# Performance work log

Hardware: AMD Instinct MI355X
Metric: run time of the kernel (lower is better)

## Reference

```python
import jax, jax.numpy as jnp
import numpy as np

EPS = 1e-5
SLOPE = 0.2


def knn_feature(x, k):
    # x: (B,N,C) -> (B,N,k,2C) edge features: concat(neighbor - center, center)
    xx = jnp.sum(x * x, axis=-1)                      # (B,N)
    inner = jnp.einsum('bnc,bmc->bnm', x, x)          # (B,N,N)
    pair = 2.0 * inner - xx[:, :, None] - xx[:, None, :]  # negative squared dist
    idx = jax.lax.top_k(pair, k)[1]                   # (B,N,k) nearest neighbors
    nbr = jax.vmap(lambda xb, ib: xb[ib])(x, idx)     # (B,N,k,C) gather
    ctr = jnp.broadcast_to(x[:, :, None, :], nbr.shape)
    return jnp.concatenate([nbr - ctr, ctr], axis=-1)


def conv_bn_lrelu(h, w, g, b):
    # 1x1 conv == pointwise matmul; BN in training mode (batch stats, biased var)
    h = jnp.einsum('bnkc,oc->bnko', h, w)
    m = jnp.mean(h, axis=(0, 1, 2))
    v = jnp.mean(jnp.square(h - m), axis=(0, 1, 2))
    h = g * (h - m) * jax.lax.rsqrt(v + EPS) + b
    return jnp.where(h >= 0, h, SLOPE * h)


def setup_inputs() -> dict:
    key = jax.random.key(0)
    B, N, C, K, H, O = 4, 4096, 3, 20, 64, 64
    ks = jax.random.split(key, 10)
    x = jax.random.normal(ks[0], (B, N, C), dtype=jnp.float32)
    def w(kk, o, i):
        return jax.random.normal(kk, (o, i), dtype=jnp.float32) * (1.0 / np.sqrt(i))
    return {
        'x': x,
        'w1': w(ks[1], H, 2 * C),
        'w2': w(ks[2], H, H),
        'w3': w(ks[3], H, H),
        'w4': w(ks[4], H, 2 * H),
        'w5': w(ks[5], H, H),
        'w6': w(ks[6], H, H),
        'w7': w(ks[7], H, 2 * H),
        'w8': w(ks[8], H, H),
        'w9': w(ks[9], O, H),
        'gamma': jnp.ones((9, H), dtype=jnp.float32),
        'beta': jnp.zeros((9, H), dtype=jnp.float32),
        'k': 20,
    }


def reference(x, w1, w2, w3, w4, w5, w6, w7, w8, w9, gamma, beta, k):
    h = knn_feature(x, k)                      # (B,N,k,6)
    h = conv_bn_lrelu(h, w1, gamma[0], beta[0])
    h = conv_bn_lrelu(h, w2, gamma[1], beta[1])
    h = conv_bn_lrelu(h, w3, gamma[2], beta[2])
    x1 = jnp.max(h, axis=2)                    # (B,N,64)
    h = knn_feature(x1, k)                     # (B,N,k,128)
    h = conv_bn_lrelu(h, w4, gamma[3], beta[3])
    h = conv_bn_lrelu(h, w5, gamma[4], beta[4])
    h = conv_bn_lrelu(h, w6, gamma[5], beta[5])
    x2 = jnp.max(h, axis=2)                    # (B,N,64)
    h = knn_feature(x2, k)                     # (B,N,k,128)
    h = conv_bn_lrelu(h, w7, gamma[6], beta[6])
    h = conv_bn_lrelu(h, w8, gamma[7], beta[7])
    h = conv_bn_lrelu(h, w9, gamma[8], beta[8])
    x3 = jnp.max(h, axis=2)                    # (B,N,out_features)
    return x3
```

## Files before the change

### kernel.cpp

```cpp
#include <hip/hip_runtime.h>

namespace {

constexpr int Bc   = 4;
constexpr int Nc   = 4096;
constexpr int Kc   = 20;
constexpr int BNc  = Bc * Nc;
constexpr int PIXc = BNc * Kc;
constexpr float  NEGINF = -3.0e38f;
constexpr double EPSD   = (double)1e-5f;

template<int C>
__global__ __launch_bounds__(256)
void compute_xx_xla(const float* __restrict__ X, float* __restrict__ xxf) {
    int i = blockIdx.x * 256 + threadIdx.x;
    if (i >= BNc) return;
    const float* xp = X + (size_t)i * C;
    if constexpr (C == 3) {
        const float q0 = __fmul_rn(xp[0], xp[0]);
        const float q1 = __fmul_rn(xp[1], xp[1]);
        const float q2 = __fmul_rn(xp[2], xp[2]);
        xxf[i] = __fadd_rn(__fadd_rn(q0, q1), q2);
    } else {
        float acc[16];
#pragma unroll
        for (int l = 0; l < 16; ++l) acc[l] = 0.f;
#pragma unroll
        for (int blk = 0; blk < 4; ++blk)
#pragma unroll
            for (int l = 0; l < 16; ++l)
                acc[l] = __fadd_rn(acc[l], __fmul_rn(xp[blk * 16 + l], xp[blk * 16 + l]));
        float a8[8];
#pragma unroll
        for (int l = 0; l < 8; ++l) a8[l] = __fadd_rn(acc[l], acc[l + 8]);
        float a4[4];
#pragma unroll
        for (int l = 0; l < 4; ++l) a4[l] = __fadd_rn(a8[l], a8[l + 4]);
        xxf[i] = __fadd_rn(__fadd_rn(a4[0], a4[2]), __fadd_rn(a4[1], a4[3]));
    }
}

template<int C>
__global__ __launch_bounds__(256)
void pair_tile(const float* __restrict__ X, const float* __restrict__ xxf,
               float* __restrict__ S, int b) {
    constexpr int P = C + 1;
    __shared__ float sxn[64 * P], sxm[64 * P];
    __shared__ float sxxn[64], sxxm[64];
    const int tid = threadIdx.x;
    const int tn  = blockIdx.x >> 6;
    const int tm  = blockIdx.x & 63;
    const float* Xn = X + ((size_t)b * Nc + tn * 64) * C;
    const float* Xm = X + ((size_t)b * Nc + tm * 64) * C;
    for (int f = tid; f < 64 * C; f += 256) {
        const int row = f / C, c = f - row * C;
        sxn[row * P + c] = Xn[f];
        sxm[row * P + c] = Xm[f];
    }
    if (tid < 64)        sxxn[tid]      = xxf[b * Nc + tn * 64 + tid];
    else if (tid < 128)  sxxm[tid - 64] = xxf[b * Nc + tm * 64 + (tid - 64)];
    __syncthreads();

    const int rn0 = (tid >> 4) * 4;
    const int rm0 = (tid & 15) * 4;
    float a00=0,a01=0,a02=0,a03=0, a10=0,a11=0,a12=0,a13=0;
    float a20=0,a21=0,a22=0,a23=0, a30=0,a31=0,a32=0,a33=0;
#pragma unroll 4
    for (int c = 0; c < C; ++c) {
        const float n0 = sxn[(rn0    ) * P + c];
        const float n1 = sxn[(rn0 + 1) * P + c];
        const float n2 = sxn[(rn0 + 2) * P + c];
        const float n3 = sxn[(rn0 + 3) * P + c];
        const float m0 = sxm[(rm0    ) * P + c];
        const float m1 = sxm[(rm0 + 1) * P + c];
        const float m2 = sxm[(rm0 + 2) * P + c];
        const float m3 = sxm[(rm0 + 3) * P + c];
        a00 = __builtin_fmaf(n0, m0, a00); a01 = __builtin_fmaf(n0, m1, a01);
        a02 = __builtin_fmaf(n0, m2, a02); a03 = __builtin_fmaf(n0, m3, a03);
        a10 = __builtin_fmaf(n1, m0, a10); a11 = __builtin_fmaf(n1, m1, a11);
        a12 = __builtin_fmaf(n1, m2, a12); a13 = __builtin_fmaf(n1, m3, a13);
        a20 = __builtin_fmaf(n2, m0, a20); a21 = __builtin_fmaf(n2, m1, a21);
        a22 = __builtin_fmaf(n2, m2, a22); a23 = __builtin_fmaf(n2, m3, a23);
        a30 = __builtin_fmaf(n3, m0, a30); a31 = __builtin_fmaf(n3, m1, a31);
        a32 = __builtin_fmaf(n3, m2, a32); a33 = __builtin_fmaf(n3, m3, a33);
    }
    const float xm0 = sxxm[rm0], xm1 = sxxm[rm0 + 1], xm2 = sxxm[rm0 + 2], xm3 = sxxm[rm0 + 3];
#define PAIR_ROW(i, r0, r1, r2, r3)                                                     \
    {                                                                                   \
        const float xn_ = sxxn[rn0 + i];                                                \
        float4 v;                                                                       \
        v.x = __fsub_rn(__fsub_rn(__fmul_rn(2.0f, r0), xn_), xm0);                      \
        v.y = __fsub_rn(__fsub_rn(__fmul_rn(2.0f, r1), xn_), xm1);                      \
        v.z = __fsub_rn(__fsub_rn(__fmul_rn(2.0f, r2), xn_), xm2);                      \
        v.w = __fsub_rn(__fsub_rn(__fmul_rn(2.0f, r3), xn_), xm3);                      \
        *(float4*)&S[(size_t)(tn * 64 + rn0 + i) * Nc + tm * 64 + rm0] = v;             \
    }
    PAIR_ROW(0, a00, a01, a02, a03)
    PAIR_ROW(1, a10, a11, a12, a13)
    PAIR_ROW(2, a20, a21, a22, a23)
    PAIR_ROW(3, a30, a31, a32, a33)
#undef PAIR_ROW
}

__global__ __launch_bounds__(256)
void brute_select(const float* __restrict__ S, int* __restrict__ knnIdx, int b) {
    const int lane = threadIdx.x & 63;
    const int wv   = threadIdx.x >> 6;
    const int n    = blockIdx.x * 4 + wv;
    const float* Sr = S + (size_t)n * Nc;
    float v[64];
#pragma unroll
    for (int j = 0; j < 64; ++j) v[j] = Sr[j * 64 + lane];
    int* outp = knnIdx + ((size_t)b * Nc + n) * Kc;
    for (int round = 0; round < Kc; ++round) {
        float bv = NEGINF; int bi = 0x7fffffff;
#pragma unroll
        for (int j = 0; j < 64; ++j) {
            const int mi = j * 64 + lane;
            const bool better = (v[j] > bv) || (v[j] == bv && mi < bi);
            bv = better ? v[j] : bv;
            bi = better ? mi : bi;
        }
#pragma unroll
        for (int s = 1; s < 64; s <<= 1) {
            const float ov = __shfl_xor(bv, s);
            const int   oi = __shfl_xor(bi, s);
            const bool better = (ov > bv) || (ov == bv && oi < bi);
            bv = better ? ov : bv;
            bi = better ? oi : bi;
        }
        if (lane == 0) outp[round] = bi;
#pragma unroll
        for (int j = 0; j < 64; ++j)
            if (j == (bi >> 6) && (bi & 63) == lane) v[j] = NEGINF;
    }
}

__device__ __forceinline__ float bn_lrelu_np(float hv, float m, float r,
                                             float g, float bb) {
    float t = __fsub_rn(hv, m);
    t = __fmul_rn(g, t);
    t = __fmul_rn(t, r);
    t = __fadd_rn(t, bb);
    return t >= 0.f ? t : __fmul_rn(0.2f, t);
}

__global__ __launch_bounds__(256)
void edge_conv3(const float* __restrict__ X, const int* __restrict__ knn,
                const float* __restrict__ W, float* __restrict__ h) {
    constexpr int F = 6, PW = 8, TP = 64;
    __shared__ float sA[TP * PW];
    __shared__ float sWT[F * 65];
    const int tid = threadIdx.x;
    for (int f = tid; f < 64 * F; f += 256) {
        const int o = f & 63, cc = f >> 6;
        sWT[cc * 65 + o] = W[o * F + cc];
    }
    const int pix0 = blockIdx.x * TP;
    for (int f = tid; f < TP * F; f += 256) {
        const int pix = f / F, c = f - pix * F;
        const int p  = pix0 + pix;
        const int bn = p / Kc;
        const int b  = bn >> 12;
        const int j  = knn[p];
        float v;
        if (c < 3) v = __fsub_rn(X[((size_t)(b << 12) + j) * 3 + c],
                                 X[(size_t)bn * 3 + c]);
        else       v = X[(size_t)bn * 3 + (c - 3)];
        sA[pix * PW + c] = v;
    }
    __syncthreads();
    const int ty = tid >> 4, tx = tid & 15;
    const int p0 = ty * 4, o0 = tx * 4;
    float acc[4][4];
#pragma unroll
    for (int i = 0; i < 4; ++i)
#pragma unroll
        for (int j = 0; j < 4; ++j) acc[i][j] = 0.f;
#pragma unroll
    for (int c = 0; c < F; ++c) {
        float av[4], wv[4];
#pragma unroll
        for (int i = 0; i < 4; ++i) av[i] = sA[(p0 + i) * PW + c];
#pragma unroll
        for (int j = 0; j < 4; ++j) wv[j] = sWT[c * 65 + o0 + j];
#pragma unroll
        for (int i = 0; i < 4; ++i)
#pragma unroll
            for (int j = 0; j < 4; ++j)
                acc[i][j] = __builtin_fmaf(av[i], wv[j], acc[i][j]);
    }
#pragma unroll
    for (int i = 0; i < 4; ++i)
        *(float4*)&h[(size_t)(pix0 + p0 + i) * 64 + o0] =
            make_float4(acc[i][0], acc[i][1], acc[i][2], acc[i][3]);
}

__global__ __launch_bounds__(256)
void edge_conv64(const float* __restrict__ X, const int* __restrict__ knn,
                 const float* __restrict__ W, float* __restrict__ h) {
    constexpr int F = 128, TP = 64, PW = 129;
    __shared__ float sA[TP * PW];
    __shared__ float sWT[64 * 65];
    const int tid = threadIdx.x;
    const int pix0 = blockIdx.x * TP;
    for (int f = tid; f < TP * F; f += 256) {
        const int pix = f >> 7, c = f & 127;
        const int p  = pix0 + pix;
        const int bn = p / Kc;
        const int b  = bn >> 12;
        const int j  = knn[p];
        float v;
        if (c < 64) v = __fsub_rn(X[((size_t)(b << 12) + j) * 64 + c],
                                  X[(size_t)bn * 64 + c]);
        else        v = X[(size_t)bn * 64 + (c - 64)];
        sA[pix * PW + c] = v;
    }
    const int ty = tid >> 4, tx = tid & 15;
    const int p0 = ty * 4, o0 = tx * 4;
    float acc[4][4];
#pragma unroll
    for (int i = 0; i < 4; ++i)
#pragma unroll
        for (int j = 0; j < 4; ++j) acc[i][j] = 0.f;
#pragma unroll
    for (int ph = 0; ph < 2; ++ph) {
        for (int f = tid; f < 4096; f += 256) {
            const int o = f & 63, cc = f >> 6;
            sWT[cc * 65 + o] = W[o * F + ph * 64 + cc];
        }
        __syncthreads();
#pragma unroll 2
        for (int cc = 0; cc < 64; ++cc) {
            const int c = ph * 64 + cc;
            float av[4], wv[4];
#pragma unroll
            for (int i = 0; i < 4; ++i) av[i] = sA[(p0 + i) * PW + c];
#pragma unroll
            for (int j = 0; j < 4; ++j) wv[j] = sWT[cc * 65 + o0 + j];
#pragma unroll
            for (int i = 0; i < 4; ++i)
#pragma unroll
                for (int j = 0; j < 4; ++j)
                    acc[i][j] = __builtin_fmaf(av[i], wv[j], acc[i][j]);
        }
        __syncthreads();
    }
#pragma unroll
    for (int i = 0; i < 4; ++i)
        *(float4*)&h[(size_t)(pix0 + p0 + i) * 64 + o0] =
            make_float4(acc[i][0], acc[i][1], acc[i][2], acc[i][3]);
}

__global__ __launch_bounds__(256)
void hidden_conv_tile(float* __restrict__ h, const float* __restrict__ W,
                      const float* __restrict__ mr, const float* __restrict__ g,
                      const float* __restrict__ bt) {
    __shared__ float sA[128 * 65];
    __shared__ float sWT[64 * 68];
    const int tid = threadIdx.x;
    for (int f = tid; f < 4096; f += 256) {
        const int o = f & 63, c = f >> 6;
        sWT[c * 68 + o] = W[o * 64 + c];
    }
    const size_t pix0 = (size_t)blockIdx.x * 128;
    for (int f = tid; f < 128 * 64; f += 256) {
        const int pix = f >> 6, c = f & 63;
        const float hv = h[(pix0 + pix) * 64 + c];
        sA[pix * 65 + c] = bn_lrelu_np(hv, mr[c], mr[64 + c], g[c], bt[c]);
    }
    __syncthreads();

    const int ty = tid >> 4, tx = tid & 15;
    const int p0 = ty * 8, o0 = tx * 4;
    float acc[8][4];
#pragma unroll
    for (int i = 0; i < 8; ++i)
#pragma unroll
        for (int j = 0; j < 4; ++j) acc[i][j] = 0.f;
#pragma unroll 2
    for (int c = 0; c < 64; ++c) {
        const float4 wv = *(const float4*)&sWT[c * 68 + o0];
        float av[8];
#pragma unroll
        for (int i = 0; i < 8; ++i) av[i] = sA[(p0 + i) * 65 + c];
#pragma unroll
        for (int i = 0; i < 8; ++i) {
            acc[i][0] = __builtin_fmaf(av[i], wv.x, acc[i][0]);
            acc[i][1] = __builtin_fmaf(av[i], wv.y, acc[i][1]);
            acc[i][2] = __builtin_fmaf(av[i], wv.z, acc[i][2]);
            acc[i][3] = __builtin_fmaf(av[i], wv.w, acc[i][3]);
        }
    }
#pragma unroll
    for (int i = 0; i < 8; ++i)
        *(float4*)&h[(pix0 + p0 + i) * 64 + o0] =
            make_float4(acc[i][0], acc[i][1], acc[i][2], acc[i][3]);
}

__global__ __launch_bounds__(256)
void maxk_np(const float* __restrict__ h, const float* __restrict__ mr,
             const float* __restrict__ g, const float* __restrict__ bt,
             float* __restrict__ out) {
    const int i  = blockIdx.x * 256 + threadIdx.x;
    const int o  = i & 63;
    const int bn = i >> 6;
    const float m = mr[o], r = mr[64 + o], gg = g[o], bb = bt[o];
    const float* hp = h + (size_t)bn * Kc * 64 + o;
    float mx = NEGINF;
#pragma unroll
    for (int k = 0; k < Kc; ++k) mx = fmaxf(mx, bn_lrelu_np(hp[k * 64], m, r, gg, bb));
    out[i] = mx;
}

__global__ __launch_bounds__(256)
void stats64(const float* __restrict__ h, double* __restrict__ stats) {
    __shared__ double sp[4 * 128];
    const int tid = threadIdx.x, o = tid & 63, w = tid >> 6;
    double s1 = 0.0, s2 = 0.0;
    for (int p = blockIdx.x * 4 + w; p < PIXc; p += 4096) {
        const double d = (double)h[(size_t)p * 64 + o];
        s1 += d; s2 += d * d;
    }
    sp[w * 128 + o]      = s1;
    sp[w * 128 + 64 + o] = s2;
    __syncthreads();
    if (tid < 128) {
        const double s = sp[tid] + sp[128 + tid] + sp[256 + tid] + sp[384 + tid];
        atomicAdd(&stats[tid], s);
    }
}

__global__ void finalize_f(const double* __restrict__ stats, float* __restrict__ mr) {
    const int o = threadIdx.x;
    const double inv  = 1.0 / (double)PIXc;
    const double mean = stats[o] * inv;
    const double var  = stats[64 + o] * inv - mean * mean;
    mr[o]      = (float)mean;
    mr[64 + o] = (float)(1.0 / sqrt(var + EPSD));
}

}

extern "C" void kernel_launch(void* const* d_in, const int* in_sizes, int n_in,
                              void* d_out, int out_size, void* d_ws, size_t ws_size,
                              hipStream_t stream) {
    (void)in_sizes; (void)n_in; (void)out_size; (void)ws_size;
    const float* x     = (const float*)d_in[0];
    const float* w[9]  = {(const float*)d_in[1], (const float*)d_in[2], (const float*)d_in[3],
                          (const float*)d_in[4], (const float*)d_in[5], (const float*)d_in[6],
                          (const float*)d_in[7], (const float*)d_in[8], (const float*)d_in[9]};
    const float* gamma = (const float*)d_in[10];
    const float* beta  = (const float*)d_in[11];
    float* out = (float*)d_out;

    double* statsD = (double*)d_ws;
    float*  mr     = (float*)(statsD + 9 * 128);
    float*  xxf    = mr + 9 * 128;
    int*  knnIdx   = (int*)(xxf + BNc);
    float* x1      = (float*)(knnIdx + PIXc);
    float* x2      = x1 + (size_t)BNc * 64;
    float* h       = x2 + (size_t)BNc * 64;
    float* S       = h;

    hipMemsetAsync(statsD, 0, 9 * 128 * sizeof(double), stream);

#define BN_STATS(L) \
    stats64<<<1024, 256, 0, stream>>>(h, statsD + (L) * 128); \
    finalize_f<<<1, 64, 0, stream>>>(statsD + (L) * 128, mr + (L) * 128)

    compute_xx_xla<3><<<64, 256, 0, stream>>>(x, xxf);
    for (int b = 0; b < Bc; ++b) {
        pair_tile<3><<<4096, 256, 0, stream>>>(x, xxf, S, b);
        brute_select<<<1024, 256, 0, stream>>>(S, knnIdx, b);
    }
    edge_conv3<<<PIXc / 64, 256, 0, stream>>>(x, knnIdx, w[0], h);
    BN_STATS(0);
    hidden_conv_tile<<<PIXc / 128, 256, 0, stream>>>(h, w[1], mr + 0 * 128, gamma + 0 * 64, beta + 0 * 64);
    BN_STATS(1);
    hidden_conv_tile<<<PIXc / 128, 256, 0, stream>>>(h, w[2], mr + 1 * 128, gamma + 1 * 64, beta + 1 * 64);
    BN_STATS(2);
    maxk_np<<<4096, 256, 0, stream>>>(h, mr + 2 * 128, gamma + 2 * 64, beta + 2 * 64, x1);

    compute_xx_xla<64><<<64, 256, 0, stream>>>(x1, xxf);
    for (int b = 0; b < Bc; ++b) {
        pair_tile<64><<<4096, 256, 0, stream>>>(x1, xxf, S, b);
        brute_select<<<1024, 256, 0, stream>>>(S, knnIdx, b);
    }
    edge_conv64<<<PIXc / 64, 256, 0, stream>>>(x1, knnIdx, w[3], h);
    BN_STATS(3);
    hidden_conv_tile<<<PIXc / 128, 256, 0, stream>>>(h, w[4], mr + 3 * 128, gamma + 3 * 64, beta + 3 * 64);
    BN_STATS(4);
    hidden_conv_tile<<<PIXc / 128, 256, 0, stream>>>(h, w[5], mr + 4 * 128, gamma + 4 * 64, beta + 4 * 64);
    BN_STATS(5);
    maxk_np<<<4096, 256, 0, stream>>>(h, mr + 5 * 128, gamma + 5 * 64, beta + 5 * 64, x2);

    compute_xx_xla<64><<<64, 256, 0, stream>>>(x2, xxf);
    for (int b = 0; b < Bc; ++b) {
        pair_tile<64><<<4096, 256, 0, stream>>>(x2, xxf, S, b);
        brute_select<<<1024, 256, 0, stream>>>(S, knnIdx, b);
    }
    edge_conv64<<<PIXc / 64, 256, 0, stream>>>(x2, knnIdx, w[6], h);
    BN_STATS(6);
    hidden_conv_tile<<<PIXc / 128, 256, 0, stream>>>(h, w[7], mr + 6 * 128, gamma + 6 * 64, beta + 6 * 64);
    BN_STATS(7);
    hidden_conv_tile<<<PIXc / 128, 256, 0, stream>>>(h, w[8], mr + 7 * 128, gamma + 7 * 64, beta + 7 * 64);
    BN_STATS(8);
    maxk_np<<<4096, 256, 0, stream>>>(h, mr + 8 * 128, gamma + 8 * 64, beta + 8 * 64, out);
#undef BN_STATS
}
```

Before: 3.562 ms.

## Fuse BatchNorm statistics reduction into conv kernel epilogues and retile conv outputs

Removes the standalone stats64 pass and computes per-channel sum and sum-of-squares in double inside the edge and hidden conv kernels. The reduction uses wave shuffles, then shared memory, then one atomicAdd per channel per block. The conv thread tiles also change to 8 output channels per thread with float4 weight loads, and shared memory is reused for the partial sums. This avoids re-reading the large activation buffer once per layer, at the cost of double-precision shuffles and more atomics in every conv block.

Result: faster. 3.426 ms, median of 2 (-3.8%).

```diff
diff --git a/kernel.cpp b/kernel.cpp
--- a/kernel.cpp
+++ b/kernel.cpp
@@ -147,14 +147,16 @@
 
 __global__ __launch_bounds__(256)
 void edge_conv3(const float* __restrict__ X, const int* __restrict__ knn,
-                const float* __restrict__ W, float* __restrict__ h) {
+                const float* __restrict__ W, float* __restrict__ h,
+                double* __restrict__ stats) {
     constexpr int F = 6, PW = 8, TP = 64;
     __shared__ float sA[TP * PW];
     __shared__ float sWT[F * 65];
+    __shared__ double sp[4 * 128];
     const int tid = threadIdx.x;
     for (int f = tid; f < 64 * F; f += 256) {
-        const int o = f & 63, cc = f >> 6;
-        sWT[cc * 65 + o] = W[o * F + cc];
+        const int o = f / F, cc = f - o * F;
+        sWT[cc * 65 + o] = W[f];
     }
     const int pix0 = blockIdx.x * TP;
     for (int f = tid; f < TP * F; f += 256) {
@@ -194,17 +196,47 @@
     for (int i = 0; i < 4; ++i)
         *(float4*)&h[(size_t)(pix0 + p0 + i) * 64 + o0] =
             make_float4(acc[i][0], acc[i][1], acc[i][2], acc[i][3]);
+    double s1[4], s2[4];
+#pragma unroll
+    for (int j = 0; j < 4; ++j) { s1[j] = 0.0; s2[j] = 0.0; }
+#pragma unroll
+    for (int i = 0; i < 4; ++i)
+#pragma unroll
+        for (int j = 0; j < 4; ++j) {
+            const double d = (double)acc[i][j];
+            s1[j] += d; s2[j] += d * d;
+        }
+#pragma unroll
+    for (int mask = 16; mask <= 32; mask <<= 1)
+#pragma unroll
+        for (int j = 0; j < 4; ++j) {
+            s1[j] += __shfl_xor(s1[j], mask);
+            s2[j] += __shfl_xor(s2[j], mask);
+        }
+    if ((tid & 48) == 0) {
+        const int w = tid >> 6;
+#pragma unroll
+        for (int j = 0; j < 4; ++j) {
+            sp[w * 128 + o0 + j]      = s1[j];
+            sp[w * 128 + 64 + o0 + j] = s2[j];
+        }
+    }
+    __syncthreads();
+    if (tid < 128)
+        atomicAdd(&stats[tid], sp[tid] + sp[128 + tid] + sp[256 + tid] + sp[384 + tid]);
 }
 
 __global__ __launch_bounds__(256)
 void edge_conv64(const float* __restrict__ X, const int* __restrict__ knn,
-                 const float* __restrict__ W, float* __restrict__ h) {
-    constexpr int F = 128, TP = 64, PW = 129;
-    __shared__ float sA[TP * PW];
-    __shared__ float sWT[64 * 65];
+                 const float* __restrict__ W, float* __restrict__ h,
+                 double* __restrict__ stats) {
+    __shared__ alignas(16) float smem[64 * 129 + 64 * 68];
+    float*  sA  = smem;
+    float*  sWT = smem + 64 * 129;
+    double* sp  = (double*)smem;
     const int tid = threadIdx.x;
-    const int pix0 = blockIdx.x * TP;
-    for (int f = tid; f < TP * F; f += 256) {
+    const int pix0 = blockIdx.x * 64;
+    for (int f = tid; f < 8192; f += 256) {
         const int pix = f >> 7, c = f & 127;
         const int p  = pix0 + pix;
         const int bn = p / Kc;
@@ -214,88 +246,159 @@
         if (c < 64) v = __fsub_rn(X[((size_t)(b << 12) + j) * 64 + c],
                                   X[(size_t)bn * 64 + c]);
         else        v = X[(size_t)bn * 64 + (c - 64)];
-        sA[pix * PW + c] = v;
-    }
-    const int ty = tid >> 4, tx = tid & 15;
-    const int p0 = ty * 4, o0 = tx * 4;
-    float acc[4][4];
-#pragma unroll
-    for (int i = 0; i < 4; ++i)
-#pragma unroll
-        for (int j = 0; j < 4; ++j) acc[i][j] = 0.f;
+        sA[pix * 129 + c] = v;
+    }
+    const int og = tid & 7, pg = tid >> 3;
+    const int p0 = pg * 2, o0 = og * 8;
+    float acc[2][8];
+#pragma unroll
+    for (int i = 0; i < 2; ++i)
+#pragma unroll
+        for (int j = 0; j < 8; ++j) acc[i][j] = 0.f;
 #pragma unroll
     for (int ph = 0; ph < 2; ++ph) {
         for (int f = tid; f < 4096; f += 256) {
-            const int o = f & 63, cc = f >> 6;
-            sWT[cc * 65 + o] = W[o * F + ph * 64 + cc];
+            const int o = f >> 6, cc = f & 63;
+            sWT[cc * 68 + o] = W[o * 128 + ph * 64 + cc];
         }
         __syncthreads();
 #pragma unroll 2
         for (int cc = 0; cc < 64; ++cc) {
             const int c = ph * 64 + cc;
-            float av[4], wv[4];
-#pragma unroll
-            for (int i = 0; i < 4; ++i) av[i] = sA[(p0 + i) * PW + c];
-#pragma unroll
-            for (int j = 0; j < 4; ++j) wv[j] = sWT[cc * 65 + o0 + j];
-#pragma unroll
-            for (int i = 0; i < 4; ++i)
-#pragma unroll
-                for (int j = 0; j < 4; ++j)
-                    acc[i][j] = __builtin_fmaf(av[i], wv[j], acc[i][j]);
+            const float4 w0 = *(const float4*)&sWT[cc * 68 + o0];
+            const float4 w1 = *(const float4*)&sWT[cc * 68 + o0 + 4];
+            const float a0 = sA[(p0    ) * 129 + c];
+            const float a1 = sA[(p0 + 1) * 129 + c];
+            acc[0][0] = __builtin_fmaf(a0, w0.x, acc[0][0]); acc[0][1] = __builtin_fmaf(a0, w0.y, acc[0][1]);
+            acc[0][2] = __builtin_fmaf(a0, w0.z, acc[0][2]); acc[0][3] = __builtin_fmaf(a0, w0.w, acc[0][3]);
+            acc[0][4] = __builtin_fmaf(a0, w1.x, acc[0][4]); acc[0][5] = __builtin_fmaf(a0, w1.y, acc[0][5]);
+            acc[0][6] = __builtin_fmaf(a0, w1.z, acc[0][6]); acc[0][7] = __builtin_fmaf(a0, w1.w, acc[0][7]);
+            acc[1][0] = __builtin_fmaf(a1, w0.x, acc[1][0]); acc[1][1] = __builtin_fmaf(a1, w0.y, acc[1][1]);
+            acc[1][2] = __builtin_fmaf(a1, w0.z, acc[1][2]); acc[1][3] = __builtin_fmaf(a1, w0.w, acc[1][3]);
+            acc[1][4] = __builtin_fmaf(a1, w1.x, acc[1][4]); acc[1][5] = __builtin_fmaf(a1, w1.y, acc[1][5]);
+            acc[1][6] = __builtin_fmaf(a1, w1.z, acc[1][6]); acc[1][7] = __builtin_fmaf(a1, w1.w, acc[1][7]);
         }
         __syncthreads();
     }
 #pragma unroll
-    for (int i = 0; i < 4; ++i)
-        *(float4*)&h[(size_t)(pix0 + p0 + i) * 64 + o0] =
-            make_float4(acc[i][0], acc[i][1], acc[i][2], acc[i][3]);
+    for (int i = 0; i < 2; ++i) {
+        float* dst = &h[(size_t)(pix0 + p0 + i) * 64 + o0];
+        *(float4*)dst       = make_float4(acc[i][0], acc[i][1], acc[i][2], acc[i][3]);
+        *(float4*)(dst + 4) = make_float4(acc[i][4], acc[i][5], acc[i][6], acc[i][7]);
+    }
+    double s1[8], s2[8];
+#pragma unroll
+    for (int j = 0; j < 8; ++j) { s1[j] = 0.0; s2[j] = 0.0; }
+#pragma unroll
+    for (int i = 0; i < 2; ++i)
+#pragma unroll
+        for (int j = 0; j < 8; ++j) {
+            const double d = (double)acc[i][j];
+            s1[j] += d; s2[j] += d * d;
+        }
+#pragma unroll
+    for (int mask = 8; mask <= 32; mask <<= 1)
+#pragma unroll
+        for (int j = 0; j < 8; ++j) {
+            s1[j] += __shfl_xor(s1[j], mask);
+            s2[j] += __shfl_xor(s2[j], mask);
+        }
+    __syncthreads();
+    if ((tid & 56) == 0) {
+        const int w = tid >> 6;
+#pragma unroll
+        for (int j = 0; j < 8; ++j) {
+            sp[w * 128 + o0 + j]      = s1[j];
+            sp[w * 128 + 64 + o0 + j] = s2[j];
+        }
+    }
+    __syncthreads();
+    if (tid < 128)
+        atomicAdd(&stats[tid], sp[tid] + sp[128 + tid] + sp[256 + tid] + sp[384 + tid]);
 }
 
 __global__ __launch_bounds__(256)
 void hidden_conv_tile(float* __restrict__ h, const float* __restrict__ W,
                       const float* __restrict__ mr, const float* __restrict__ g,
-                      const float* __restrict__ bt) {
-    __shared__ float sA[128 * 65];
-    __shared__ float sWT[64 * 68];
+                      const float* __restrict__ bt, double* __restrict__ stats) {
+    __shared__ alignas(16) float smem[128 * 65 + 64 * 68];
+    float*  sA  = smem;
+    float*  sWT = smem + 128 * 65;
+    double* sp  = (double*)smem;
     const int tid = threadIdx.x;
     for (int f = tid; f < 4096; f += 256) {
-        const int o = f & 63, c = f >> 6;
-        sWT[c * 68 + o] = W[o * 64 + c];
+        const int o = f >> 6, c = f & 63;
+        sWT[c * 68 + o] = W[f];
     }
     const size_t pix0 = (size_t)blockIdx.x * 128;
-    for (int f = tid; f < 128 * 64; f += 256) {
+    for (int f = tid; f < 8192; f += 256) {
         const int pix = f >> 6, c = f & 63;
         const float hv = h[(pix0 + pix) * 64 + c];
         sA[pix * 65 + c] = bn_lrelu_np(hv, mr[c], mr[64 + c], g[c], bt[c]);
     }
     __syncthreads();
 
-    const int ty = tid >> 4, tx = tid & 15;
-    const int p0 = ty * 8, o0 = tx * 4;
-    float acc[8][4];
-#pragma unroll
-    for (int i = 0; i < 8; ++i)
-#pragma unroll
-        for (int j = 0; j < 4; ++j) acc[i][j] = 0.f;
+    const int og = tid & 7, pg = tid >> 3;
+    const int p0 = pg * 4, o0 = og * 8;
+    float acc[4][8];
+#pragma unroll
+    for (int i = 0; i < 4; ++i)
+#pragma unroll
+        for (int j = 0; j < 8; ++j) acc[i][j] = 0.f;
 #pragma unroll 2
     for (int c = 0; c < 64; ++c) {
-        const float4 wv = *(const float4*)&sWT[c * 68 + o0];
-        float av[8];
-#pragma unroll
-        for (int i = 0; i < 8; ++i) av[i] = sA[(p0 + i) * 65 + c];
-#pragma unroll
-        for (int i = 0; i < 8; ++i) {
-            acc[i][0] = __builtin_fmaf(av[i], wv.x, acc[i][0]);
-            acc[i][1] = __builtin_fmaf(av[i], wv.y, acc[i][1]);
-            acc[i][2] = __builtin_fmaf(av[i], wv.z, acc[i][2]);
-            acc[i][3] = __builtin_fmaf(av[i], wv.w, acc[i][3]);
-        }
-    }
-#pragma unroll
-    for (int i = 0; i < 8; ++i)
-        *(float4*)&h[(pix0 + p0 + i) * 64 + o0] =
-            make_float4(acc[i][0], acc[i][1], acc[i][2], acc[i][3]);
+        const float4 w0 = *(const float4*)&sWT[c * 68 + o0];
+        const float4 w1 = *(const float4*)&sWT[c * 68 + o0 + 4];
+        float av[4];
+#pragma unroll
+        for (int i = 0; i < 4; ++i) av[i] = sA[(p0 + i) * 65 + c];
+#pragma unroll
+        for (int i = 0; i < 4; ++i) {
+            acc[i][0] = __builtin_fmaf(av[i], w0.x, acc[i][0]);
+            acc[i][1] = __builtin_fmaf(av[i], w0.y, acc[i][1]);
+            acc[i][2] = __builtin_fmaf(av[i], w0.z, acc[i][2]);
+            acc[i][3] = __builtin_fmaf(av[i], w0.w, acc[i][3]);
+            acc[i][4] = __builtin_fmaf(av[i], w1.x, acc[i][4]);
+            acc[i][5] = __builtin_fmaf(av[i], w1.y, acc[i][5]);
+            acc[i][6] = __builtin_fmaf(av[i], w1.z, acc[i][6]);
+            acc[i][7] = __builtin_fmaf(av[i], w1.w, acc[i][7]);
+        }
+    }
+#pragma unroll
+    for (int i = 0; i < 4; ++i) {
+        float* dst = &h[(pix0 + p0 + i) * 64 + o0];
+        *(float4*)dst       = make_float4(acc[i][0], acc[i][1], acc[i][2], acc[i][3]);
+        *(float4*)(dst + 4) = make_float4(acc[i][4], acc[i][5], acc[i][6], acc[i][7]);
+    }
+    double s1[8], s2[8];
+#pragma unroll
+    for (int j = 0; j < 8; ++j) { s1[j] = 0.0; s2[j] = 0.0; }
+#pragma unroll
+    for (int i = 0; i < 4; ++i)
+#pragma unroll
+        for (int j = 0; j < 8; ++j) {
+            const double d = (double)acc[i][j];
+            s1[j] += d; s2[j] += d * d;
+        }
+#pragma unroll
+    for (int mask = 8; mask <= 32; mask <<= 1)
+#pragma unroll
+        for (int j = 0; j < 8; ++j) {
+            s1[j] += __shfl_xor(s1[j], mask);
+            s2[j] += __shfl_xor(s2[j], mask);
+        }
+    __syncthreads();
+    if ((tid & 56) == 0) {
+        const int w = tid >> 6;
+#pragma unroll
+        for (int j = 0; j < 8; ++j) {
+            sp[w * 128 + o0 + j]      = s1[j];
+            sp[w * 128 + 64 + o0 + j] = s2[j];
+        }
+    }
+    __syncthreads();
+    if (tid < 128)
+        atomicAdd(&stats[tid], sp[tid] + sp[128 + tid] + sp[256 + tid] + sp[384 + tid]);
 }
 
 __global__ __launch_bounds__(256)
@@ -311,24 +414,6 @@
 #pragma unroll
     for (int k = 0; k < Kc; ++k) mx = fmaxf(mx, bn_lrelu_np(hp[k * 64], m, r, gg, bb));
     out[i] = mx;
-}
-
-__global__ __launch_bounds__(256)
-void stats64(const float* __restrict__ h, double* __restrict__ stats) {
-    __shared__ double sp[4 * 128];
-    const int tid = threadIdx.x, o = tid & 63, w = tid >> 6;
-    double s1 = 0.0, s2 = 0.0;
-    for (int p = blockIdx.x * 4 + w; p < PIXc; p += 4096) {
-        const double d = (double)h[(size_t)p * 64 + o];
-        s1 += d; s2 += d * d;
-    }
-    sp[w * 128 + o]      = s1;
-    sp[w * 128 + 64 + o] = s2;
-    __syncthreads();
-    if (tid < 128) {
-        const double s = sp[tid] + sp[128 + tid] + sp[256 + tid] + sp[384 + tid];
-        atomicAdd(&stats[tid], s);
-    }
 }
 
 __global__ void finalize_f(const double* __restrict__ stats, float* __restrict__ mr) {
@@ -365,21 +450,17 @@
 
     hipMemsetAsync(statsD, 0, 9 * 128 * sizeof(double), stream);
 
-#define BN_STATS(L) \
-    stats64<<<1024, 256, 0, stream>>>(h, statsD + (L) * 128); \
-    finalize_f<<<1, 64, 0, stream>>>(statsD + (L) * 128, mr + (L) * 128)
-
     compute_xx_xla<3><<<64, 256, 0, stream>>>(x, xxf);
     for (int b = 0; b < Bc; ++b) {
         pair_tile<3><<<4096, 256, 0, stream>>>(x, xxf, S, b);
         brute_select<<<1024, 256, 0, stream>>>(S, knnIdx, b);
     }
-    edge_conv3<<<PIXc / 64, 256, 0, stream>>>(x, knnIdx, w[0], h);
-    BN_STATS(0);
-    hidden_conv_tile<<<PIXc / 128, 256, 0, stream>>>(h, w[1], mr + 0 * 128, gamma + 0 * 64, beta + 0 * 64);
-    BN_STATS(1);
-    hidden_conv_tile<<<PIXc / 128, 256, 0, stream>>>(h, w[2], mr + 1 * 128, gamma + 1 * 64, beta + 1 * 64);
-    BN_STATS(2);
+    edge_conv3<<<PIXc / 64, 256, 0, stream>>>(x, knnIdx, w[0], h, statsD + 0 * 128);
+    finalize_f<<<1, 64, 0, stream>>>(statsD + 0 * 128, mr + 0 * 128);
+    hidden_conv_tile<<<PIXc / 128, 256, 0, stream>>>(h, w[1], mr + 0 * 128, gamma + 0 * 64, beta + 0 * 64, statsD + 1 * 128);
+    finalize_f<<<1, 64, 0, stream>>>(statsD + 1 * 128, mr + 1 * 128);
+    hidden_conv_tile<<<PIXc / 128, 256, 0, stream>>>(h, w[2], mr + 1 * 128, gamma + 1 * 64, beta + 1 * 64, statsD + 2 * 128);
+    finalize_f<<<1, 64, 0, stream>>>(statsD + 2 * 128, mr + 2 * 128);
     maxk_np<<<4096, 256, 0, stream>>>(h, mr + 2 * 128, gamma + 2 * 64, beta + 2 * 64, x1);
 
     compute_xx_xla<64><<<64, 256, 0, stream>>>(x1, xxf);
@@ -387,12 +468,12 @@
         pair_tile<64><<<4096, 256, 0, stream>>>(x1, xxf, S, b);
         brute_select<<<1024, 256, 0, stream>>>(S, knnIdx, b);
     }
-    edge_conv64<<<PIXc / 64, 256, 0, stream>>>(x1, knnIdx, w[3], h);
-    BN_STATS(3);
-    hidden_conv_tile<<<PIXc / 128, 256, 0, stream>>>(h, w[4], mr + 3 * 128, gamma + 3 * 64, beta + 3 * 64);
-    BN_STATS(4);
-    hidden_conv_tile<<<PIXc / 128, 256, 0, stream>>>(h, w[5], mr + 4 * 128, gamma + 4 * 64, beta + 4 * 64);
-    BN_STATS(5);
+    edge_conv64<<<PIXc / 64, 256, 0, stream>>>(x1, knnIdx, w[3], h, statsD + 3 * 128);
+    finalize_f<<<1, 64, 0, stream>>>(statsD + 3 * 128, mr + 3 * 128);
+    hidden_conv_tile<<<PIXc / 128, 256, 0, stream>>>(h, w[4], mr + 3 * 128, gamma + 3 * 64, beta + 3 * 64, statsD + 4 * 128);
+    finalize_f<<<1, 64, 0, stream>>>(statsD + 4 * 128, mr + 4 * 128);
+    hidden_conv_tile<<<PIXc / 128, 256, 0, stream>>>(h, w[5], mr + 4 * 128, gamma + 4 * 64, beta + 4 * 64, statsD + 5 * 128);
+    finalize_f<<<1, 64, 0, stream>>>(statsD + 5 * 128, mr + 5 * 128);
     maxk_np<<<4096, 256, 0, stream>>>(h, mr + 5 * 128, gamma + 5 * 64, beta + 5 * 64, x2);
 
     compute_xx_xla<64><<<64, 256, 0, stream>>>(x2, xxf);
@@ -400,12 +481,11 @@
         pair_tile<64><<<4096, 256, 0, stream>>>(x2, xxf, S, b);
         brute_select<<<1024, 256, 0, stream>>>(S, knnIdx, b);
     }
-    edge_conv64<<<PIXc / 64, 256, 0, stream>>>(x2, knnIdx, w[6], h);
-    BN_STATS(6);
-    hidden_conv_tile<<<PIXc / 128, 256, 0, stream>>>(h, w[7], mr + 6 * 128, gamma + 6 * 64, beta + 6 * 64);
-    BN_STATS(7);
-    hidden_conv_tile<<<PIXc / 128, 256, 0, stream>>>(h, w[8], mr + 7 * 128, gamma + 7 * 64, beta + 7 * 64);
-    BN_STATS(8);
+    edge_conv64<<<PIXc / 64, 256, 0, stream>>>(x2, knnIdx, w[6], h, statsD + 6 * 128);
+    finalize_f<<<1, 64, 0, stream>>>(statsD + 6 * 128, mr + 6 * 128);
+    hidden_conv_tile<<<PIXc / 128, 256, 0, stream>>>(h, w[7], mr + 6 * 128, gamma + 6 * 64, beta + 6 * 64, statsD + 7 * 128);
+    finalize_f<<<1, 64, 0, stream>>>(statsD + 7 * 128, mr + 7 * 128);
+    hidden_conv_tile<<<PIXc / 128, 256, 0, stream>>>(h, w[8], mr + 7 * 128, gamma + 7 * 64, beta + 7 * 64, statsD + 8 * 128);
+    finalize_f<<<1, 64, 0, stream>>>(statsD + 8 * 128, mr + 8 * 128);
     maxk_np<<<4096, 256, 0, stream>>>(h, mr + 8 * 128, gamma + 8 * 64, beta + 8 * 64, out);
-#undef BN_STATS
-}
+}
```
